# Kernel optimization log

Measured on AMD Instinct MI355X. Metric: run time of the kernel, lower is better.

Reference implementation:

```python
import jax, jax.numpy as jnp
import numpy as np

N, L, S, E, A, D = 16, 256, 128, 128, 9, 768
ARG_ROLES = 23      # score width = ARG_ROLES + 1
MAX_ARG = 9         # hard-coded max_len_arg in the torch module
N_HID = 768


def setup_inputs() -> dict:
    key = jax.random.key(0)
    ks = jax.random.split(key, 10)
    all_embeddings = jax.random.normal(ks[0], (N, L, D), jnp.float32)
    # last-3-layer BERT attention maps, 12 heads, positive entries
    attn_last3 = jax.random.uniform(ks[1], (3, N, 12, L, L), jnp.float32)
    # per-sample sorted distinct first-subword indices (all positive, full length:
    # the ragged filter idxs>0 then keeps everything -> fixed-shape gather)
    idx_keys = jax.random.split(ks[2], N)
    cand = jnp.arange(1, L - MAX_ARG - 1)
    idxs_to_collect = jax.vmap(
        lambda k: jnp.sort(jax.random.choice(k, cand, (S + 2,), replace=False))
    )(idx_keys).astype(jnp.int32)
    is_triggers = (jax.random.uniform(ks[3], (N, S)) < 0.05).astype(jnp.float32)
    is_triggers = is_triggers.at[:, 0].set(1.0)  # >=1 trigger per sample
    entity_mapping = jax.random.normal(ks[4], (N, S, E), jnp.float32) * 0.05
    arg_weight_matrices = jax.random.normal(ks[5], (N, MAX_ARG, A), jnp.float32) * 0.3
    map_keys = jax.random.split(ks[6], N)
    arg_mapping = jax.vmap(
        lambda k: jax.random.permutation(k, ARG_ROLES + 1)[:A]
    )(map_keys).astype(jnp.int32)
    W1 = jax.random.normal(ks[7], (6 * D, N_HID), jnp.float32) * 0.02
    b1 = jnp.zeros((N_HID,), jnp.float32)
    W2 = jax.random.normal(ks[8], (N_HID, 1), jnp.float32) * 0.02
    b2 = jnp.zeros((1,), jnp.float32)
    return {
        "all_embeddings": all_embeddings,
        "attn_last3": attn_last3,
        "entity_mapping": entity_mapping,
        "arg_weight_matrices": arg_weight_matrices,
        "is_triggers": is_triggers,
        "W1": W1, "b1": b1, "W2": W2, "b2": b2,
        "idxs_to_collect": idxs_to_collect,
        "arg_mapping": arg_mapping,
    }


def reference(all_embeddings, attn_last3, entity_mapping, arg_weight_matrices,
              is_triggers, W1, b1, W2, b2, idxs_to_collect, arg_mapping):
    sqrt_d = jnp.sqrt(jnp.asarray(D, jnp.float32))
    sent_idx = idxs_to_collect[:, :S]                      # [N,S] first-subword ids
    # get_fist_subword_embeddings: ragged gather (full-length here)
    sent_emb = jnp.take_along_axis(all_embeddings, sent_idx[:, :, None], axis=1)  # [N,S,D]
    # arg-type tokens sit right after the second-to-last [SEP]
    arg_pos = idxs_to_collect[:, -2:-1] + 1 + jnp.arange(MAX_ARG)[None, :]        # [N,9]
    arg_raw = jnp.take_along_axis(all_embeddings, arg_pos[:, :, None], axis=1)    # [N,9,D]

    entity_emb = jnp.einsum('nsd,nse->ned', sent_emb, entity_mapping)             # [N,E,D]
    trig = jnp.sum(sent_emb * is_triggers[..., None], axis=1) \
           / jnp.sum(is_triggers, axis=1, keepdims=True)                          # [N,D]
    del trig  # _trigger is computed but unused downstream in the torch forward
    arg_emb = jnp.einsum('nkd,nka->nad', arg_raw, arg_weight_matrices)            # [N,A,D]

    # bi-attention scores (broadcast-mul-sum == contraction over D)
    t2a = jnp.einsum('ned,nad->nea', entity_emb, arg_emb) / sqrt_d
    w = (t2a - 5.0) / 2.0                                                         # [N,E,A]
    token_argAwared = jnp.einsum('nea,nad->ned', w, arg_emb)                      # [N,E,D]
    arg_tokenAwared = jnp.einsum('nea,ned->nad', w, entity_emb)                   # [N,A,D]

    # select_hidden_att for each of the last 3 layers
    att_mean = jnp.mean(attn_last3, axis=2)                                       # [3,N,L,L]
    def sel_layer(a):  # a: [N,L,L] -> row/col gather + row renorm
        s = jax.vmap(lambda m, i: m[i][:, i])(a, sent_idx)                        # [N,S,S]
        return s / (jnp.sum(s, axis=-1, keepdims=True) + 1e-9)
    t2t = (sel_layer(att_mean[0]) + sel_layer(att_mean[1]) + sel_layer(att_mean[2])) / 3.0

    h2h_sent = jnp.einsum('nst,ntd->nsd', t2t, sent_emb)                          # [N,S,D]
    # A_h2h and H_ are projected from sent space (S) to entity space (E)
    A_h2h_e = jnp.einsum('nsd,nse->ned', h2h_sent, entity_mapping)                # [N,E,D]
    H_e = entity_emb                                                              # sent_emb projected == entity_emb

    a2a = jax.nn.softmax(jnp.einsum('nad,nbd->nab', arg_emb, arg_emb), axis=-1)   # [N,A,A]
    u2u = jnp.einsum('nab,nbd->nad', a2a, arg_emb)                                # [N,A,D]

    shp = (N, E, A, D)
    H_    = jnp.broadcast_to(H_e[:, :, None, :], shp)
    U_    = jnp.broadcast_to(arg_emb[:, None, :, :], shp)
    A_h2u = jnp.broadcast_to(token_argAwared[:, :, None, :], shp)
    A_h2h = jnp.broadcast_to(A_h2h_e[:, :, None, :], shp)
    A_u2h = jnp.broadcast_to(arg_tokenAwared[:, None, :, :], shp)
    A_u2u = jnp.broadcast_to(u2u[:, None, :, :], shp)
    latent = jnp.concatenate([H_, U_, A_h2u, A_h2h, A_u2h, A_u2u], axis=-1)       # [N,E,A,6D]

    hid = jax.nn.gelu(latent @ W1 + b1, approximate=False)                        # [N,E,A,768]
    score = (hid @ W2 + b2)[..., 0]                                               # [N,E,A]

    # map_arg_to_ids: scatter each arg slot back to its global role id
    def scatter_one(s, ids):  # s [E,A], ids [A]
        return jnp.full((E, ARG_ROLES + 1), -1e6, jnp.float32).at[:, ids].set(s)
    new_score = jax.vmap(scatter_one)(score, arg_mapping)                         # [N,E,24]
    return new_score
```

## Files before the change

kernel.cpp:

```cpp
#include <hip/hip_runtime.h>
#include <math.h>

namespace {
constexpr int N_ = 16, L_ = 256, S_ = 128, E_ = 128, A_ = 9, D_ = 768, H_ = 768, RO_ = 24;
constexpr int IDXW = 130;
constexpr int W1R = 6 * D_;
constexpr float INV_SQRT_D = 0.03608439182435161f;
}

using bshort8 = __attribute__((ext_vector_type(8))) short;
using f32x4v = __attribute__((ext_vector_type(4))) float;

__device__ __forceinline__ unsigned short f2bf(float f) {
    unsigned u = __builtin_bit_cast(unsigned, f);
    return (unsigned short)((u + 0x7fffu + ((u >> 16) & 1u)) >> 16);
}

__global__ __launch_bounds__(256) void zero2_k(float* __restrict__ Pe, float* __restrict__ Pa) {
    const int i = blockIdx.x * 256 + threadIdx.x;
    const float4 z = {0.f, 0.f, 0.f, 0.f};
    if (i < (N_ * E_ * H_) / 4) reinterpret_cast<float4*>(Pe)[i] = z;
    if (i < (N_ * A_ * H_) / 4) reinterpret_cast<float4*>(Pa)[i] = z;
}

__global__ __launch_bounds__(256) void gatherT_k(const float* __restrict__ all_emb,
                                                 const int* __restrict__ idxs,
                                                 unsigned short* __restrict__ sentT) {
    const int n = blockIdx.x, d0 = blockIdx.y * 64;
    __shared__ unsigned short tile[64][132];
#pragma unroll
    for (int it = 0; it < 8; ++it) {
        const int lin = threadIdx.x + 256 * it;
        const int s = lin >> 4, dq = (lin & 15) * 4;
        const int row = idxs[n * IDXW + s];
        const float4 v = *reinterpret_cast<const float4*>(all_emb + ((size_t)(n * L_ + row)) * D_ + d0 + dq);
        tile[dq + 0][s] = f2bf(v.x); tile[dq + 1][s] = f2bf(v.y);
        tile[dq + 2][s] = f2bf(v.z); tile[dq + 3][s] = f2bf(v.w);
    }
    __syncthreads();
#pragma unroll
    for (int it = 0; it < 8; ++it) {
        const int lin = threadIdx.x + 256 * it;
        const int d = lin >> 5, s4 = (lin & 31) * 4;
        ushort4 v = {tile[d][s4], tile[d][s4 + 1], tile[d][s4 + 2], tile[d][s4 + 3]};
        *reinterpret_cast<ushort4*>(sentT + ((size_t)(n * D_) + d0 + d) * S_ + s4) = v;
    }
}

__global__ __launch_bounds__(256) void entmapT_k(const float* __restrict__ ent_map,
                                                 unsigned short* __restrict__ entmapT) {
    const int n = blockIdx.x;
    __shared__ unsigned short tile[128][132];
#pragma unroll
    for (int it = 0; it < 16; ++it) {
        const int lin = threadIdx.x + 256 * it;
        const int s = lin >> 5, eq = (lin & 31) * 4;
        const float4 v = *reinterpret_cast<const float4*>(ent_map + ((size_t)(n * S_ + s)) * E_ + eq);
        tile[eq + 0][s] = f2bf(v.x); tile[eq + 1][s] = f2bf(v.y);
        tile[eq + 2][s] = f2bf(v.z); tile[eq + 3][s] = f2bf(v.w);
    }
    __syncthreads();
#pragma unroll
    for (int it = 0; it < 16; ++it) {
        const int lin = threadIdx.x + 256 * it;
        const int e = lin >> 5, s4 = (lin & 31) * 4;
        ushort4 v = {tile[e][s4], tile[e][s4 + 1], tile[e][s4 + 2], tile[e][s4 + 3]};
        *reinterpret_cast<ushort4*>(entmapT + ((size_t)(n * E_) + e) * S_ + s4) = v;
    }
}

__global__ __launch_bounds__(256) void transpose_w1_k(const float* __restrict__ W1, short* __restrict__ W1t) {
    __shared__ float tile[64][65];
    const int k0 = blockIdx.x * 64, h0 = blockIdx.y * 64;
    const int tx = threadIdx.x & 63, ty = threadIdx.x >> 6;
#pragma unroll
    for (int i = 0; i < 16; ++i) {
        const int r = ty + i * 4;
        tile[r][tx] = W1[(size_t)(k0 + r) * H_ + h0 + tx];
    }
    __syncthreads();
#pragma unroll
    for (int i = 0; i < 16; ++i) {
        const int r = ty + i * 4;
        W1t[(size_t)(h0 + r) * W1R + k0 + tx] = (short)f2bf(tile[tx][r]);
    }
}

__global__ __launch_bounds__(128) void t2t_k(const float* __restrict__ attn,
                                             const int* __restrict__ idxs,
                                             unsigned short* __restrict__ t2tbf) {
    const int n = blockIdx.x >> 7, s = blockIdx.x & 127;
    const int t = threadIdx.x;
    const int w = t >> 6, lane = t & 63;
    const int is = idxs[n * IDXW + s], it = idxs[n * IDXW + t];
    __shared__ float sum2[3][2][256];
    __shared__ float part[3][2];
#pragma unroll
    for (int l = 0; l < 3; ++l) {
        const float* base = attn + ((size_t)((l * N_ + n) * 12 + w * 6)) * (L_ * L_)
                          + (size_t)is * L_ + lane * 4;
        float4 acc = {0.f, 0.f, 0.f, 0.f};
#pragma unroll
        for (int h = 0; h < 6; ++h) {
            const float4 v = *reinterpret_cast<const float4*>(base + (size_t)h * (L_ * L_));
            acc.x += v.x; acc.y += v.y; acc.z += v.z; acc.w += v.w;
        }
        *reinterpret_cast<float4*>(&sum2[l][w][lane * 4]) = acc;
    }
    __syncthreads();
    float m[3];
#pragma unroll
    for (int l = 0; l < 3; ++l) {
        m[l] = (sum2[l][0][it] + sum2[l][1][it]) * (1.0f / 12.0f);
        float r = m[l];
#pragma unroll
        for (int off = 32; off; off >>= 1) r += __shfl_xor(r, off, 64);
        if (lane == 0) part[l][w] = r;
    }
    __syncthreads();
    float out = 0.f;
#pragma unroll
    for (int l = 0; l < 3; ++l)
        out += m[l] / (part[l][0] + part[l][1] + 1e-9f);
    t2tbf[((size_t)(n * S_ + s)) * S_ + t] = f2bf(out * (1.0f / 3.0f));
}

__global__ __launch_bounds__(256) void arg_u2u_k(const float* __restrict__ all_emb,
                                                 const int* __restrict__ idxs,
                                                 const float* __restrict__ argw,
                                                 float* __restrict__ argE,
                                                 unsigned short* __restrict__ argEbf,
                                                 unsigned short* __restrict__ u2ubf) {
    const int n = blockIdx.x, tid = threadIdx.x;
    __shared__ float wsm[A_][A_];
    __shared__ float part[45][4];
    __shared__ float Psm[A_][A_];
    if (tid < A_ * A_) wsm[tid / A_][tid % A_] = argw[n * A_ * A_ + tid];
    __syncthreads();
    const int p0 = idxs[n * IDXW + S_] + 1;
    float pp[45] = {};
    float vals[3][A_];
#pragma unroll
    for (int c = 0; c < 3; ++c) {
        const int d = tid + 256 * c;
        float raw[A_];
#pragma unroll
        for (int k = 0; k < A_; ++k) raw[k] = all_emb[((size_t)(n * L_ + p0 + k)) * D_ + d];
#pragma unroll
        for (int a = 0; a < A_; ++a) {
            float acc = 0.f;
#pragma unroll
            for (int k = 0; k < A_; ++k) acc = fmaf(raw[k], wsm[k][a], acc);
            vals[c][a] = acc;
            argE[((size_t)(n * A_ + a)) * D_ + d] = acc;
            argEbf[((size_t)(n * A_ + a)) * D_ + d] = f2bf(acc);
        }
        int p = 0;
#pragma unroll
        for (int a = 0; a < A_; ++a)
#pragma unroll
            for (int b = a; b < A_; ++b) pp[p++] += vals[c][a] * vals[c][b];
    }
    const int lane = tid & 63, wv = tid >> 6;
#pragma unroll
    for (int p = 0; p < 45; ++p) {
        float v = pp[p];
        for (int off = 32; off; off >>= 1) v += __shfl_down(v, off, 64);
        if (lane == 0) part[p][wv] = v;
    }
    __syncthreads();
    if (tid < 45) part[tid][0] = part[tid][0] + part[tid][1] + part[tid][2] + part[tid][3];
    __syncthreads();
    if (tid < A_) {
        const int a = tid;
        float v[A_], mx = -1e30f;
#pragma unroll
        for (int b = 0; b < A_; ++b) {
            const int lo = a < b ? a : b, hi = a < b ? b : a;
            v[b] = part[lo * (19 - lo) / 2 + hi - lo][0];
            mx = fmaxf(mx, v[b]);
        }
        float s = 0.f;
#pragma unroll
        for (int b = 0; b < A_; ++b) { v[b] = expf(v[b] - mx); s += v[b]; }
        const float inv = 1.0f / s;
#pragma unroll
        for (int b = 0; b < A_; ++b) Psm[a][b] = v[b] * inv;
    }
    __syncthreads();
#pragma unroll
    for (int c = 0; c < 3; ++c) {
        const int d = tid + 256 * c;
#pragma unroll
        for (int a = 0; a < A_; ++a) {
            float acc = 0.f;
#pragma unroll
            for (int b = 0; b < A_; ++b) acc = fmaf(Psm[a][b], vals[c][b], acc);
            u2ubf[((size_t)(n * A_ + a)) * D_ + d] = f2bf(acc);
        }
    }
}

template <int MODE>
__global__ __launch_bounds__(256) void gemm128_k(const unsigned short* __restrict__ Ab,
                                                 const unsigned short* __restrict__ BTb,
                                                 float* __restrict__ Cf,
                                                 unsigned short* __restrict__ Cb) {
    __shared__ __align__(16) short As[128][40];
    __shared__ __align__(16) short Bs[64][40];
    const int n = blockIdx.y, c0 = blockIdx.x * 64;
    const unsigned short* A = Ab + (size_t)n * S_ * S_;
    const unsigned short* BT = BTb + (size_t)n * D_ * S_;
    const int tid = threadIdx.x;
    const int wave = tid >> 6, lane = tid & 63;
    const int row16 = lane & 15, quad = lane >> 4;
    f32x4v acc[2][4] = {};
    for (int k0 = 0; k0 < S_; k0 += 32) {
#pragma unroll
        for (int i = 0; i < 2; ++i) {
            const int idx = tid + 256 * i;
            const int r = idx >> 2, q = idx & 3;
            *reinterpret_cast<bshort8*>(&As[r][q * 8]) =
                *reinterpret_cast<const bshort8*>(A + (size_t)r * S_ + k0 + q * 8);
        }
        {
            const int col = tid >> 2, q = tid & 3;
            *reinterpret_cast<bshort8*>(&Bs[col][q * 8]) =
                *reinterpret_cast<const bshort8*>(BT + (size_t)(c0 + col) * S_ + k0 + q * 8);
        }
        __syncthreads();
        bshort8 a[2], b[4];
#pragma unroll
        for (int mi = 0; mi < 2; ++mi)
            a[mi] = *reinterpret_cast<const bshort8*>(&As[wave * 32 + mi * 16 + row16][quad * 8]);
#pragma unroll
        for (int ni = 0; ni < 4; ++ni)
            b[ni] = *reinterpret_cast<const bshort8*>(&Bs[ni * 16 + row16][quad * 8]);
#pragma unroll
        for (int mi = 0; mi < 2; ++mi)
#pragma unroll
            for (int ni = 0; ni < 4; ++ni)
                acc[mi][ni] = __builtin_amdgcn_mfma_f32_16x16x32_bf16(a[mi], b[ni], acc[mi][ni], 0, 0, 0);
        __syncthreads();
    }
#pragma unroll
    for (int mi = 0; mi < 2; ++mi) {
#pragma unroll
        for (int ni = 0; ni < 4; ++ni) {
            const int rbase = wave * 32 + mi * 16 + quad * 4;
            const int col = c0 + ni * 16 + row16;
            if (MODE == 1) {
                ushort4 v = {f2bf(acc[mi][ni][0]), f2bf(acc[mi][ni][1]),
                             f2bf(acc[mi][ni][2]), f2bf(acc[mi][ni][3])};
                *reinterpret_cast<ushort4*>(Cb + (size_t)n * D_ * S_ + (size_t)col * S_ + rbase) = v;
            } else {
#pragma unroll
                for (int t = 0; t < 4; ++t) {
                    const size_t o = ((size_t)n * S_ + rbase + t) * D_ + col;
                    Cb[o] = f2bf(acc[mi][ni][t]);
                }
            }
        }
    }
}

__global__ __launch_bounds__(256) void gemm_pair_k(const unsigned short* __restrict__ t2tbf,
                                                   const unsigned short* __restrict__ entmapT,
                                                   const unsigned short* __restrict__ sentT,
                                                   float* __restrict__ entf,
                                                   unsigned short* __restrict__ entbf,
                                                   unsigned short* __restrict__ h2hT) {
    __shared__ __align__(16) short As[128][40];
    __shared__ __align__(16) short Bs[64][40];
    const int n = blockIdx.y, c0 = blockIdx.x * 64, z = blockIdx.z;
    const unsigned short* A = (z == 0 ? t2tbf : entmapT) + (size_t)n * S_ * S_;
    const unsigned short* BT = sentT + (size_t)n * D_ * S_;
    const int tid = threadIdx.x;
    const int wave = tid >> 6, lane = tid & 63;
    const int row16 = lane & 15, quad = lane >> 4;
    f32x4v acc[2][4] = {};
    for (int k0 = 0; k0 < S_; k0 += 32) {
#pragma unroll
        for (int i = 0; i < 2; ++i) {
            const int idx = tid + 256 * i;
            const int r = idx >> 2, q = idx & 3;
            *reinterpret_cast<bshort8*>(&As[r][q * 8]) =
                *reinterpret_cast<const bshort8*>(A + (size_t)r * S_ + k0 + q * 8);
        }
        {
            const int col = tid >> 2, q = tid & 3;
            *reinterpret_cast<bshort8*>(&Bs[col][q * 8]) =
                *reinterpret_cast<const bshort8*>(BT + (size_t)(c0 + col) * S_ + k0 + q * 8);
        }
        __syncthreads();
        bshort8 a[2], b[4];
#pragma unroll
        for (int mi = 0; mi < 2; ++mi)
            a[mi] = *reinterpret_cast<const bshort8*>(&As[wave * 32 + mi * 16 + row16][quad * 8]);
#pragma unroll
        for (int ni = 0; ni < 4; ++ni)
            b[ni] = *reinterpret_cast<const bshort8*>(&Bs[ni * 16 + row16][quad * 8]);
#pragma unroll
        for (int mi = 0; mi < 2; ++mi)
#pragma unroll
            for (int ni = 0; ni < 4; ++ni)
                acc[mi][ni] = __builtin_amdgcn_mfma_f32_16x16x32_bf16(a[mi], b[ni], acc[mi][ni], 0, 0, 0);
        __syncthreads();
    }
#pragma unroll
    for (int mi = 0; mi < 2; ++mi) {
#pragma unroll
        for (int ni = 0; ni < 4; ++ni) {
            const int rbase = wave * 32 + mi * 16 + quad * 4;
            const int col = c0 + ni * 16 + row16;
            if (z == 0) {
                ushort4 v = {f2bf(acc[mi][ni][0]), f2bf(acc[mi][ni][1]),
                             f2bf(acc[mi][ni][2]), f2bf(acc[mi][ni][3])};
                *reinterpret_cast<ushort4*>(h2hT + (size_t)n * D_ * S_ + (size_t)col * S_ + rbase) = v;
            } else {
#pragma unroll
                for (int t = 0; t < 4; ++t) {
                    const size_t o = ((size_t)n * S_ + rbase + t) * D_ + col;
                    entf[o] = acc[mi][ni][t];
                    entbf[o] = f2bf(acc[mi][ni][t]);
                }
            }
        }
    }
}

__global__ __launch_bounds__(256) void w_tokA_k(const float* __restrict__ ent, const float* __restrict__ argE,
                                                float* __restrict__ wbuf, unsigned short* __restrict__ tokAbf) {
    const int n = blockIdx.x >> 7, e = blockIdx.x & 127;
    const int tid = threadIdx.x;
    const float* er = ent + ((size_t)(n * E_ + e)) * D_;
    const float* ar = argE + (size_t)n * A_ * D_;
    float acc[A_] = {};
    for (int d = tid; d < D_; d += 256) {
        const float ev = er[d];
#pragma unroll
        for (int a = 0; a < A_; ++a) acc[a] = fmaf(ev, ar[(size_t)a * D_ + d], acc[a]);
    }
    const int lane = tid & 63, wv = tid >> 6;
#pragma unroll
    for (int a = 0; a < A_; ++a)
        for (int off = 32; off; off >>= 1) acc[a] += __shfl_down(acc[a], off, 64);
    __shared__ float part[A_][4];
    __shared__ float wl[A_];
    if (lane == 0)
        for (int a = 0; a < A_; ++a) part[a][wv] = acc[a];
    __syncthreads();
    if (tid < A_) {
        const float s = part[tid][0] + part[tid][1] + part[tid][2] + part[tid][3];
        const float w = (s * INV_SQRT_D - 5.0f) * 0.5f;
        wl[tid] = w;
        wbuf[(size_t)(n * E_ + e) * A_ + tid] = w;
    }
    __syncthreads();
    for (int d = tid; d < D_; d += 256) {
        float s = 0.f;
#pragma unroll
        for (int a = 0; a < A_; ++a) s = fmaf(wl[a], ar[(size_t)a * D_ + d], s);
        tokAbf[((size_t)(n * E_ + e)) * D_ + d] = f2bf(s);
    }
}

__global__ __launch_bounds__(256) void argT_k(const float* __restrict__ wbuf, const float* __restrict__ ent,
                                              unsigned short* __restrict__ argTbf) {
    const int n = blockIdx.x / A_, a = blockIdx.x % A_;
    const int tid = threadIdx.x;
    __shared__ float wl[E_];
    if (tid < E_) wl[tid] = wbuf[(size_t)(n * E_ + tid) * A_ + a];
    __syncthreads();
    const float* eb = ent + (size_t)n * E_ * D_;
    for (int d = tid; d < D_; d += 256) {
        float acc = 0.f;
        for (int e = 0; e < E_; ++e) acc = fmaf(wl[e], eb[(size_t)e * D_ + d], acc);
        argTbf[((size_t)(n * A_ + a)) * D_ + d] = f2bf(acc);
    }
}

__global__ __launch_bounds__(256) void mfma_mlp_k(const unsigned short* __restrict__ e0,
                                                  const unsigned short* __restrict__ e1,
                                                  const unsigned short* __restrict__ e2,
                                                  const unsigned short* __restrict__ a0,
                                                  const unsigned short* __restrict__ a1,
                                                  const unsigned short* __restrict__ a2,
                                                  const short* __restrict__ W1t,
                                                  float* __restrict__ Pe, float* __restrict__ Pa) {
    __shared__ __align__(16) short As[128][40];
    __shared__ __align__(16) short Bs[64][40];
    const int bx = blockIdx.x;
    const int seg = bx % 3;
    const int blk = bx / 3;
    const bool isPa = blk >= 16;
    const unsigned short* Aseg;
    int woff;
    if (isPa) {
        Aseg = seg == 0 ? a0 : (seg == 1 ? a1 : a2);
        woff = seg == 0 ? 1 * D_ : (seg == 1 ? 4 * D_ : 5 * D_);
    } else {
        Aseg = seg == 0 ? e0 : (seg == 1 ? e1 : e2);
        woff = seg == 0 ? 0 : (seg == 1 ? 2 * D_ : 3 * D_);
    }
    const int M = isPa ? N_ * A_ : N_ * E_;
    const int r0 = (isPa ? blk - 16 : blk) * 128;
    float* C = isPa ? Pa : Pe;
    const int c0 = blockIdx.y * 64;
    const int tid = threadIdx.x;
    const int wave = tid >> 6, lane = tid & 63;
    const int row16 = lane & 15, quad = lane >> 4;
    f32x4v acc[2][4] = {};
    for (int kk = 0; kk < D_; kk += 32) {
#pragma unroll
        for (int i = 0; i < 2; ++i) {
            const int idx = tid + 256 * i;
            const int r = idx >> 2, q = idx & 3;
            bshort8 av = {};
            if (r0 + r < M) av = *reinterpret_cast<const bshort8*>(Aseg + (size_t)(r0 + r) * D_ + kk + q * 8);
            *reinterpret_cast<bshort8*>(&As[r][q * 8]) = av;
        }
        {
            const int col = tid >> 2, q = tid & 3;
            *reinterpret_cast<bshort8*>(&Bs[col][q * 8]) =
                *reinterpret_cast<const bshort8*>(W1t + (size_t)(c0 + col) * W1R + woff + kk + q * 8);
        }
        __syncthreads();
        bshort8 a[2], b[4];
#pragma unroll
        for (int mi = 0; mi < 2; ++mi)
            a[mi] = *reinterpret_cast<const bshort8*>(&As[wave * 32 + mi * 16 + row16][quad * 8]);
#pragma unroll
        for (int ni = 0; ni < 4; ++ni)
            b[ni] = *reinterpret_cast<const bshort8*>(&Bs[ni * 16 + row16][quad * 8]);
#pragma unroll
        for (int mi = 0; mi < 2; ++mi)
#pragma unroll
            for (int ni = 0; ni < 4; ++ni)
                acc[mi][ni] = __builtin_amdgcn_mfma_f32_16x16x32_bf16(a[mi], b[ni], acc[mi][ni], 0, 0, 0);
        __syncthreads();
    }
#pragma unroll
    for (int mi = 0; mi < 2; ++mi) {
#pragma unroll
        for (int ni = 0; ni < 4; ++ni) {
            const int rbase = r0 + wave * 32 + mi * 16 + quad * 4;
            const int col = c0 + ni * 16 + row16;
#pragma unroll
            for (int t = 0; t < 4; ++t)
                if (rbase + t < M) atomicAdd(&C[(size_t)(rbase + t) * H_ + col], acc[mi][ni][t]);
        }
    }
}

__global__ __launch_bounds__(256) void score_k(const float* __restrict__ Pe, const float* __restrict__ Pa,
                                               const float* __restrict__ b1, const float* __restrict__ W2,
                                               const float* __restrict__ b2, const int* __restrict__ arg_map,
                                               float* __restrict__ out) {
    const int n = blockIdx.x >> 7, e = blockIdx.x & 127;
    const int tid = threadIdx.x;
    __shared__ float paS[A_ * H_];
    __shared__ float part[A_][4];
    float* orow = out + ((size_t)(n * E_ + e)) * RO_;
    if (tid < RO_) orow[tid] = -1000000.0f;
    for (int i = tid; i < A_ * H_; i += 256) paS[i] = Pa[(size_t)n * A_ * H_ + i];
    __syncthreads();
    const float* per = Pe + ((size_t)(n * E_ + e)) * H_;
    float acc[A_] = {};
    for (int h = tid; h < H_; h += 256) {
        const float pe = per[h] + b1[h];
        const float w2 = W2[h];
#pragma unroll
        for (int a = 0; a < A_; ++a) {
            const float x = pe + paS[a * H_ + h];
            const float g = x * 0.5f * (1.0f + erff(x * 0.70710678118654752f));
            acc[a] = fmaf(g, w2, acc[a]);
        }
    }
    const int lane = tid & 63, wv = tid >> 6;
#pragma unroll
    for (int a = 0; a < A_; ++a)
        for (int off = 32; off; off >>= 1) acc[a] += __shfl_down(acc[a], off, 64);
    if (lane == 0)
        for (int a = 0; a < A_; ++a) part[a][wv] = acc[a];
    __syncthreads();
    if (tid < A_) {
        const float s = part[tid][0] + part[tid][1] + part[tid][2] + part[tid][3] + b2[0];
        orow[arg_map[n * A_ + tid]] = s;
    }
}

extern "C" void kernel_launch(void* const* d_in, const int* in_sizes, int n_in,
                              void* d_out, int out_size, void* d_ws, size_t ws_size,
                              hipStream_t stream) {
    const float* all_emb = (const float*)d_in[0];
    const float* attn    = (const float*)d_in[1];
    const float* ent_map = (const float*)d_in[2];
    const float* argw    = (const float*)d_in[3];
    const float* W1 = (const float*)d_in[5];
    const float* b1 = (const float*)d_in[6];
    const float* W2 = (const float*)d_in[7];
    const float* b2 = (const float*)d_in[8];
    const int* idxs    = (const int*)d_in[9];
    const int* arg_map = (const int*)d_in[10];
    float* out = (float*)d_out;

    float* ws = (float*)d_ws;
    float* entf = ws + 0;
    float* Pe   = ws + 1572864;
    float* argE = ws + 3145728;
    float* wbuf = ws + 3256320;
    float* Pa   = ws + 3274752;
    short*          W1t     = (short*)(ws + 3385344);
    unsigned short* sentT   = (unsigned short*)(ws + 5154816);
    unsigned short* entmapT = (unsigned short*)(ws + 5941248);
    unsigned short* t2tbf   = (unsigned short*)(ws + 6072320);
    unsigned short* argEbf  = (unsigned short*)(ws + 6127616);
    unsigned short* u2ubf   = (unsigned short*)(ws + 6182912);
    unsigned short* entbf   = (unsigned short*)(ws + 6238208);
    unsigned short* h2hT    = (unsigned short*)(ws + 7024640);
    unsigned short* Ah2hbf  = (unsigned short*)(ws + 7811072);
    unsigned short* tokAbf  = (unsigned short*)(ws + 8597504);
    unsigned short* argTbf  = (unsigned short*)(ws + 9383936);

    zero2_k<<<(N_ * E_ * H_) / 4 / 256, 256, 0, stream>>>(Pe, Pa);

    gatherT_k<<<dim3(N_, D_ / 64), 256, 0, stream>>>(all_emb, idxs, sentT);
    entmapT_k<<<N_, 256, 0, stream>>>(ent_map, entmapT);
    transpose_w1_k<<<dim3(W1R / 64, H_ / 64), 256, 0, stream>>>(W1, W1t);
    t2t_k<<<N_ * S_, 128, 0, stream>>>(attn, idxs, t2tbf);
    arg_u2u_k<<<N_, 256, 0, stream>>>(all_emb, idxs, argw, argE, argEbf, u2ubf);

    gemm_pair_k<<<dim3(D_ / 64, N_, 2), 256, 0, stream>>>(t2tbf, entmapT, sentT, entf, entbf, h2hT);
    gemm128_k<2><<<dim3(D_ / 64, N_), 256, 0, stream>>>(entmapT, h2hT, nullptr, Ah2hbf);

    w_tokA_k<<<N_ * E_, 256, 0, stream>>>(entf, argE, wbuf, tokAbf);
    argT_k<<<N_ * A_, 256, 0, stream>>>(wbuf, entf, argTbf);

    mfma_mlp_k<<<dim3(54, H_ / 64), 256, 0, stream>>>(entbf, tokAbf, Ah2hbf, argEbf, argTbf, u2ubf, W1t, Pe, Pa);

    score_k<<<N_ * E_, 256, 0, stream>>>(Pe, Pa, b1, W2, b2, arg_map, out);

    (void)in_sizes; (void)n_in; (void)out_size; (void)ws_size;
}
```

Measured before the change: 350.7 us.

## Merge preprocessing kernels into one launch and replace atomics with per-segment partials

New measurement: 318.2 us. 1.1x faster.

```diff
diff --git a/kernel.cpp b/kernel.cpp
--- a/kernel.cpp
+++ b/kernel.cpp
@@ -6,6 +6,14 @@
 constexpr int IDXW = 130;
 constexpr int W1R = 6 * D_;
 constexpr float INV_SQRT_D = 0.03608439182435161f;
+constexpr int PESZ = 2048 * 768;
+constexpr int PASZ = 144 * 768;
+constexpr int GB_GATHER = 0;
+constexpr int GB_ENTMAP = 192;
+constexpr int GB_W1T    = 208;
+constexpr int GB_T2T    = 1072;
+constexpr int GB_ARGU   = 2096;
+constexpr int GB_TOTAL  = 2112;
 }
 
 using bshort8 = __attribute__((ext_vector_type(8))) short;
@@ -16,249 +24,182 @@
     return (unsigned short)((u + 0x7fffu + ((u >> 16) & 1u)) >> 16);
 }
 
-__global__ __launch_bounds__(256) void zero2_k(float* __restrict__ Pe, float* __restrict__ Pa) {
-    const int i = blockIdx.x * 256 + threadIdx.x;
-    const float4 z = {0.f, 0.f, 0.f, 0.f};
-    if (i < (N_ * E_ * H_) / 4) reinterpret_cast<float4*>(Pe)[i] = z;
-    if (i < (N_ * A_ * H_) / 4) reinterpret_cast<float4*>(Pa)[i] = z;
-}
-
-__global__ __launch_bounds__(256) void gatherT_k(const float* __restrict__ all_emb,
-                                                 const int* __restrict__ idxs,
-                                                 unsigned short* __restrict__ sentT) {
-    const int n = blockIdx.x, d0 = blockIdx.y * 64;
-    __shared__ unsigned short tile[64][132];
-#pragma unroll
-    for (int it = 0; it < 8; ++it) {
-        const int lin = threadIdx.x + 256 * it;
-        const int s = lin >> 4, dq = (lin & 15) * 4;
-        const int row = idxs[n * IDXW + s];
-        const float4 v = *reinterpret_cast<const float4*>(all_emb + ((size_t)(n * L_ + row)) * D_ + d0 + dq);
-        tile[dq + 0][s] = f2bf(v.x); tile[dq + 1][s] = f2bf(v.y);
-        tile[dq + 2][s] = f2bf(v.z); tile[dq + 3][s] = f2bf(v.w);
-    }
-    __syncthreads();
-#pragma unroll
-    for (int it = 0; it < 8; ++it) {
-        const int lin = threadIdx.x + 256 * it;
-        const int d = lin >> 5, s4 = (lin & 31) * 4;
-        ushort4 v = {tile[d][s4], tile[d][s4 + 1], tile[d][s4 + 2], tile[d][s4 + 3]};
-        *reinterpret_cast<ushort4*>(sentT + ((size_t)(n * D_) + d0 + d) * S_ + s4) = v;
-    }
-}
-
-__global__ __launch_bounds__(256) void entmapT_k(const float* __restrict__ ent_map,
-                                                 unsigned short* __restrict__ entmapT) {
-    const int n = blockIdx.x;
-    __shared__ unsigned short tile[128][132];
-#pragma unroll
-    for (int it = 0; it < 16; ++it) {
-        const int lin = threadIdx.x + 256 * it;
-        const int s = lin >> 5, eq = (lin & 31) * 4;
-        const float4 v = *reinterpret_cast<const float4*>(ent_map + ((size_t)(n * S_ + s)) * E_ + eq);
-        tile[eq + 0][s] = f2bf(v.x); tile[eq + 1][s] = f2bf(v.y);
-        tile[eq + 2][s] = f2bf(v.z); tile[eq + 3][s] = f2bf(v.w);
-    }
-    __syncthreads();
-#pragma unroll
-    for (int it = 0; it < 16; ++it) {
-        const int lin = threadIdx.x + 256 * it;
-        const int e = lin >> 5, s4 = (lin & 31) * 4;
-        ushort4 v = {tile[e][s4], tile[e][s4 + 1], tile[e][s4 + 2], tile[e][s4 + 3]};
-        *reinterpret_cast<ushort4*>(entmapT + ((size_t)(n * E_) + e) * S_ + s4) = v;
-    }
-}
-
-__global__ __launch_bounds__(256) void transpose_w1_k(const float* __restrict__ W1, short* __restrict__ W1t) {
-    __shared__ float tile[64][65];
-    const int k0 = blockIdx.x * 64, h0 = blockIdx.y * 64;
-    const int tx = threadIdx.x & 63, ty = threadIdx.x >> 6;
-#pragma unroll
-    for (int i = 0; i < 16; ++i) {
-        const int r = ty + i * 4;
-        tile[r][tx] = W1[(size_t)(k0 + r) * H_ + h0 + tx];
-    }
-    __syncthreads();
-#pragma unroll
-    for (int i = 0; i < 16; ++i) {
-        const int r = ty + i * 4;
-        W1t[(size_t)(h0 + r) * W1R + k0 + tx] = (short)f2bf(tile[tx][r]);
-    }
-}
-
-__global__ __launch_bounds__(128) void t2t_k(const float* __restrict__ attn,
-                                             const int* __restrict__ idxs,
-                                             unsigned short* __restrict__ t2tbf) {
-    const int n = blockIdx.x >> 7, s = blockIdx.x & 127;
-    const int t = threadIdx.x;
-    const int w = t >> 6, lane = t & 63;
-    const int is = idxs[n * IDXW + s], it = idxs[n * IDXW + t];
-    __shared__ float sum2[3][2][256];
-    __shared__ float part[3][2];
-#pragma unroll
-    for (int l = 0; l < 3; ++l) {
-        const float* base = attn + ((size_t)((l * N_ + n) * 12 + w * 6)) * (L_ * L_)
-                          + (size_t)is * L_ + lane * 4;
-        float4 acc = {0.f, 0.f, 0.f, 0.f};
-#pragma unroll
-        for (int h = 0; h < 6; ++h) {
-            const float4 v = *reinterpret_cast<const float4*>(base + (size_t)h * (L_ * L_));
-            acc.x += v.x; acc.y += v.y; acc.z += v.z; acc.w += v.w;
-        }
-        *reinterpret_cast<float4*>(&sum2[l][w][lane * 4]) = acc;
-    }
-    __syncthreads();
-    float m[3];
-#pragma unroll
-    for (int l = 0; l < 3; ++l) {
-        m[l] = (sum2[l][0][it] + sum2[l][1][it]) * (1.0f / 12.0f);
-        float r = m[l];
-#pragma unroll
-        for (int off = 32; off; off >>= 1) r += __shfl_xor(r, off, 64);
-        if (lane == 0) part[l][w] = r;
-    }
-    __syncthreads();
-    float out = 0.f;
-#pragma unroll
-    for (int l = 0; l < 3; ++l)
-        out += m[l] / (part[l][0] + part[l][1] + 1e-9f);
-    t2tbf[((size_t)(n * S_ + s)) * S_ + t] = f2bf(out * (1.0f / 3.0f));
-}
-
-__global__ __launch_bounds__(256) void arg_u2u_k(const float* __restrict__ all_emb,
-                                                 const int* __restrict__ idxs,
-                                                 const float* __restrict__ argw,
-                                                 float* __restrict__ argE,
-                                                 unsigned short* __restrict__ argEbf,
-                                                 unsigned short* __restrict__ u2ubf) {
-    const int n = blockIdx.x, tid = threadIdx.x;
-    __shared__ float wsm[A_][A_];
-    __shared__ float part[45][4];
-    __shared__ float Psm[A_][A_];
-    if (tid < A_ * A_) wsm[tid / A_][tid % A_] = argw[n * A_ * A_ + tid];
-    __syncthreads();
-    const int p0 = idxs[n * IDXW + S_] + 1;
-    float pp[45] = {};
-    float vals[3][A_];
-#pragma unroll
-    for (int c = 0; c < 3; ++c) {
-        const int d = tid + 256 * c;
-        float raw[A_];
-#pragma unroll
-        for (int k = 0; k < A_; ++k) raw[k] = all_emb[((size_t)(n * L_ + p0 + k)) * D_ + d];
-#pragma unroll
-        for (int a = 0; a < A_; ++a) {
-            float acc = 0.f;
-#pragma unroll
-            for (int k = 0; k < A_; ++k) acc = fmaf(raw[k], wsm[k][a], acc);
-            vals[c][a] = acc;
-            argE[((size_t)(n * A_ + a)) * D_ + d] = acc;
-            argEbf[((size_t)(n * A_ + a)) * D_ + d] = f2bf(acc);
-        }
-        int p = 0;
-#pragma unroll
-        for (int a = 0; a < A_; ++a)
-#pragma unroll
-            for (int b = a; b < A_; ++b) pp[p++] += vals[c][a] * vals[c][b];
-    }
-    const int lane = tid & 63, wv = tid >> 6;
-#pragma unroll
-    for (int p = 0; p < 45; ++p) {
-        float v = pp[p];
-        for (int off = 32; off; off >>= 1) v += __shfl_down(v, off, 64);
-        if (lane == 0) part[p][wv] = v;
-    }
-    __syncthreads();
-    if (tid < 45) part[tid][0] = part[tid][0] + part[tid][1] + part[tid][2] + part[tid][3];
-    __syncthreads();
-    if (tid < A_) {
-        const int a = tid;
-        float v[A_], mx = -1e30f;
-#pragma unroll
-        for (int b = 0; b < A_; ++b) {
-            const int lo = a < b ? a : b, hi = a < b ? b : a;
-            v[b] = part[lo * (19 - lo) / 2 + hi - lo][0];
-            mx = fmaxf(mx, v[b]);
-        }
-        float s = 0.f;
-#pragma unroll
-        for (int b = 0; b < A_; ++b) { v[b] = expf(v[b] - mx); s += v[b]; }
-        const float inv = 1.0f / s;
-#pragma unroll
-        for (int b = 0; b < A_; ++b) Psm[a][b] = v[b] * inv;
-    }
-    __syncthreads();
-#pragma unroll
-    for (int c = 0; c < 3; ++c) {
-        const int d = tid + 256 * c;
-#pragma unroll
-        for (int a = 0; a < A_; ++a) {
-            float acc = 0.f;
-#pragma unroll
-            for (int b = 0; b < A_; ++b) acc = fmaf(Psm[a][b], vals[c][b], acc);
-            u2ubf[((size_t)(n * A_ + a)) * D_ + d] = f2bf(acc);
-        }
-    }
-}
-
-template <int MODE>
-__global__ __launch_bounds__(256) void gemm128_k(const unsigned short* __restrict__ Ab,
-                                                 const unsigned short* __restrict__ BTb,
-                                                 float* __restrict__ Cf,
-                                                 unsigned short* __restrict__ Cb) {
-    __shared__ __align__(16) short As[128][40];
-    __shared__ __align__(16) short Bs[64][40];
-    const int n = blockIdx.y, c0 = blockIdx.x * 64;
-    const unsigned short* A = Ab + (size_t)n * S_ * S_;
-    const unsigned short* BT = BTb + (size_t)n * D_ * S_;
-    const int tid = threadIdx.x;
-    const int wave = tid >> 6, lane = tid & 63;
-    const int row16 = lane & 15, quad = lane >> 4;
-    f32x4v acc[2][4] = {};
-    for (int k0 = 0; k0 < S_; k0 += 32) {
-#pragma unroll
-        for (int i = 0; i < 2; ++i) {
-            const int idx = tid + 256 * i;
-            const int r = idx >> 2, q = idx & 3;
-            *reinterpret_cast<bshort8*>(&As[r][q * 8]) =
-                *reinterpret_cast<const bshort8*>(A + (size_t)r * S_ + k0 + q * 8);
-        }
-        {
-            const int col = tid >> 2, q = tid & 3;
-            *reinterpret_cast<bshort8*>(&Bs[col][q * 8]) =
-                *reinterpret_cast<const bshort8*>(BT + (size_t)(c0 + col) * S_ + k0 + q * 8);
-        }
-        __syncthreads();
-        bshort8 a[2], b[4];
-#pragma unroll
-        for (int mi = 0; mi < 2; ++mi)
-            a[mi] = *reinterpret_cast<const bshort8*>(&As[wave * 32 + mi * 16 + row16][quad * 8]);
-#pragma unroll
-        for (int ni = 0; ni < 4; ++ni)
-            b[ni] = *reinterpret_cast<const bshort8*>(&Bs[ni * 16 + row16][quad * 8]);
-#pragma unroll
-        for (int mi = 0; mi < 2; ++mi)
-#pragma unroll
-            for (int ni = 0; ni < 4; ++ni)
-                acc[mi][ni] = __builtin_amdgcn_mfma_f32_16x16x32_bf16(a[mi], b[ni], acc[mi][ni], 0, 0, 0);
-        __syncthreads();
-    }
-#pragma unroll
-    for (int mi = 0; mi < 2; ++mi) {
-#pragma unroll
-        for (int ni = 0; ni < 4; ++ni) {
-            const int rbase = wave * 32 + mi * 16 + quad * 4;
-            const int col = c0 + ni * 16 + row16;
-            if (MODE == 1) {
-                ushort4 v = {f2bf(acc[mi][ni][0]), f2bf(acc[mi][ni][1]),
-                             f2bf(acc[mi][ni][2]), f2bf(acc[mi][ni][3])};
-                *reinterpret_cast<ushort4*>(Cb + (size_t)n * D_ * S_ + (size_t)col * S_ + rbase) = v;
-            } else {
-#pragma unroll
-                for (int t = 0; t < 4; ++t) {
-                    const size_t o = ((size_t)n * S_ + rbase + t) * D_ + col;
-                    Cb[o] = f2bf(acc[mi][ni][t]);
-                }
+__global__ __launch_bounds__(256) void stage1_k(const float* __restrict__ all_emb,
+                                                const int* __restrict__ idxs,
+                                                const float* __restrict__ ent_map,
+                                                const float* __restrict__ W1,
+                                                const float* __restrict__ argw,
+                                                const float* __restrict__ attn,
+                                                unsigned short* __restrict__ sentT,
+                                                unsigned short* __restrict__ entmapT,
+                                                short* __restrict__ W1t,
+                                                unsigned short* __restrict__ t2tbf,
+                                                float* __restrict__ argE,
+                                                unsigned short* __restrict__ argEbf,
+                                                unsigned short* __restrict__ u2ubf) {
+    __shared__ __align__(16) unsigned char smem[33792];
+    const int b = blockIdx.x, tid = threadIdx.x;
+
+    if (b < GB_ENTMAP) {
+        const int n = b / 12, d0 = (b % 12) * 64;
+        auto tile = (unsigned short (*)[132])smem;
+#pragma unroll
+        for (int it = 0; it < 8; ++it) {
+            const int lin = tid + 256 * it;
+            const int s = lin >> 4, dq = (lin & 15) * 4;
+            const int row = idxs[n * IDXW + s];
+            const float4 v = *reinterpret_cast<const float4*>(all_emb + ((size_t)(n * L_ + row)) * D_ + d0 + dq);
+            tile[dq + 0][s] = f2bf(v.x); tile[dq + 1][s] = f2bf(v.y);
+            tile[dq + 2][s] = f2bf(v.z); tile[dq + 3][s] = f2bf(v.w);
+        }
+        __syncthreads();
+#pragma unroll
+        for (int it = 0; it < 8; ++it) {
+            const int lin = tid + 256 * it;
+            const int d = lin >> 5, s4 = (lin & 31) * 4;
+            ushort4 v = {tile[d][s4], tile[d][s4 + 1], tile[d][s4 + 2], tile[d][s4 + 3]};
+            *reinterpret_cast<ushort4*>(sentT + ((size_t)(n * D_) + d0 + d) * S_ + s4) = v;
+        }
+    } else if (b < GB_W1T) {
+        const int n = b - GB_ENTMAP;
+        auto tile = (unsigned short (*)[132])smem;
+#pragma unroll
+        for (int it = 0; it < 16; ++it) {
+            const int lin = tid + 256 * it;
+            const int s = lin >> 5, eq = (lin & 31) * 4;
+            const float4 v = *reinterpret_cast<const float4*>(ent_map + ((size_t)(n * S_ + s)) * E_ + eq);
+            tile[eq + 0][s] = f2bf(v.x); tile[eq + 1][s] = f2bf(v.y);
+            tile[eq + 2][s] = f2bf(v.z); tile[eq + 3][s] = f2bf(v.w);
+        }
+        __syncthreads();
+#pragma unroll
+        for (int it = 0; it < 16; ++it) {
+            const int lin = tid + 256 * it;
+            const int e = lin >> 5, s4 = (lin & 31) * 4;
+            ushort4 v = {tile[e][s4], tile[e][s4 + 1], tile[e][s4 + 2], tile[e][s4 + 3]};
+            *reinterpret_cast<ushort4*>(entmapT + ((size_t)(n * E_) + e) * S_ + s4) = v;
+        }
+    } else if (b < GB_T2T) {
+        const int b2 = b - GB_W1T;
+        const int k0 = (b2 % 72) * 64, h0 = (b2 / 72) * 64;
+        auto tile = (float (*)[65])smem;
+        const int tx = tid & 63, ty = tid >> 6;
+#pragma unroll
+        for (int i = 0; i < 16; ++i) {
+            const int r = ty + i * 4;
+            tile[r][tx] = W1[(size_t)(k0 + r) * H_ + h0 + tx];
+        }
+        __syncthreads();
+#pragma unroll
+        for (int i = 0; i < 16; ++i) {
+            const int r = ty + i * 4;
+            W1t[(size_t)(h0 + r) * W1R + k0 + tx] = (short)f2bf(tile[tx][r]);
+        }
+    } else if (b < GB_ARGU) {
+        const int idx = b - GB_T2T;
+        const int n = idx >> 6;
+        const int half = tid >> 7, t128 = tid & 127;
+        const int s = ((idx & 63) << 1) | half;
+        const int w = t128 >> 6, lane = tid & 63;
+        float* sum2 = (float*)smem;
+        float* part = (float*)(smem + 12288);
+        const int is = idxs[n * IDXW + s], it = idxs[n * IDXW + t128];
+#pragma unroll
+        for (int l = 0; l < 3; ++l) {
+            const float* base = attn + ((size_t)((l * N_ + n) * 12 + w * 6)) * (L_ * L_)
+                              + (size_t)is * L_ + lane * 4;
+            float4 acc = {0.f, 0.f, 0.f, 0.f};
+#pragma unroll
+            for (int h = 0; h < 6; ++h) {
+                const float4 v = *reinterpret_cast<const float4*>(base + (size_t)h * (L_ * L_));
+                acc.x += v.x; acc.y += v.y; acc.z += v.z; acc.w += v.w;
+            }
+            *reinterpret_cast<float4*>(&sum2[(((half * 3 + l) * 2 + w) << 8) + lane * 4]) = acc;
+        }
+        __syncthreads();
+        float m[3];
+#pragma unroll
+        for (int l = 0; l < 3; ++l) {
+            m[l] = (sum2[(((half * 3 + l) * 2 + 0) << 8) + it] +
+                    sum2[(((half * 3 + l) * 2 + 1) << 8) + it]) * (1.0f / 12.0f);
+            float r = m[l];
+#pragma unroll
+            for (int off = 32; off; off >>= 1) r += __shfl_xor(r, off, 64);
+            if (lane == 0) part[(half * 3 + l) * 2 + w] = r;
+        }
+        __syncthreads();
+        float out = 0.f;
+#pragma unroll
+        for (int l = 0; l < 3; ++l)
+            out += m[l] / (part[(half * 3 + l) * 2 + 0] + part[(half * 3 + l) * 2 + 1] + 1e-9f);
+        t2tbf[((size_t)(n * S_ + s)) * S_ + t128] = f2bf(out * (1.0f / 3.0f));
+    } else {
+        const int n = b - GB_ARGU;
+        auto wsm = (float (*)[A_])smem;
+        auto part45 = (float (*)[4])(smem + 512);
+        auto Psm = (float (*)[A_])(smem + 1536);
+        if (tid < A_ * A_) wsm[tid / A_][tid % A_] = argw[n * A_ * A_ + tid];
+        __syncthreads();
+        const int p0 = idxs[n * IDXW + S_] + 1;
+        float pp[45] = {};
+        float vals[3][A_];
+#pragma unroll
+        for (int c = 0; c < 3; ++c) {
+            const int d = tid + 256 * c;
+            float raw[A_];
+#pragma unroll
+            for (int k = 0; k < A_; ++k) raw[k] = all_emb[((size_t)(n * L_ + p0 + k)) * D_ + d];
+#pragma unroll
+            for (int a = 0; a < A_; ++a) {
+                float acc = 0.f;
+#pragma unroll
+                for (int k = 0; k < A_; ++k) acc = fmaf(raw[k], wsm[k][a], acc);
+                vals[c][a] = acc;
+                argE[((size_t)(n * A_ + a)) * D_ + d] = acc;
+                argEbf[((size_t)(n * A_ + a)) * D_ + d] = f2bf(acc);
+            }
+            int p = 0;
+#pragma unroll
+            for (int a = 0; a < A_; ++a)
+#pragma unroll
+                for (int bb = a; bb < A_; ++bb) pp[p++] += vals[c][a] * vals[c][bb];
+        }
+        const int lane = tid & 63, wv = tid >> 6;
+#pragma unroll
+        for (int p = 0; p < 45; ++p) {
+            float v = pp[p];
+            for (int off = 32; off; off >>= 1) v += __shfl_down(v, off, 64);
+            if (lane == 0) part45[p][wv] = v;
+        }
+        __syncthreads();
+        if (tid < 45) part45[tid][0] = part45[tid][0] + part45[tid][1] + part45[tid][2] + part45[tid][3];
+        __syncthreads();
+        if (tid < A_) {
+            const int a = tid;
+            float v[A_], mx = -1e30f;
+#pragma unroll
+            for (int bb = 0; bb < A_; ++bb) {
+                const int lo = a < bb ? a : bb, hi = a < bb ? bb : a;
+                v[bb] = part45[lo * (19 - lo) / 2 + hi - lo][0];
+                mx = fmaxf(mx, v[bb]);
+            }
+            float sm = 0.f;
+#pragma unroll
+            for (int bb = 0; bb < A_; ++bb) { v[bb] = expf(v[bb] - mx); sm += v[bb]; }
+            const float inv = 1.0f / sm;
+#pragma unroll
+            for (int bb = 0; bb < A_; ++bb) Psm[a][bb] = v[bb] * inv;
+        }
+        __syncthreads();
+#pragma unroll
+        for (int c = 0; c < 3; ++c) {
+            const int d = tid + 256 * c;
+#pragma unroll
+            for (int a = 0; a < A_; ++a) {
+                float acc = 0.f;
+#pragma unroll
+                for (int bb = 0; bb < A_; ++bb) acc = fmaf(Psm[a][bb], vals[c][bb], acc);
+                u2ubf[((size_t)(n * A_ + a)) * D_ + d] = f2bf(acc);
             }
         }
     }
@@ -329,54 +270,122 @@
     }
 }
 
-__global__ __launch_bounds__(256) void w_tokA_k(const float* __restrict__ ent, const float* __restrict__ argE,
-                                                float* __restrict__ wbuf, unsigned short* __restrict__ tokAbf) {
-    const int n = blockIdx.x >> 7, e = blockIdx.x & 127;
-    const int tid = threadIdx.x;
-    const float* er = ent + ((size_t)(n * E_ + e)) * D_;
-    const float* ar = argE + (size_t)n * A_ * D_;
-    float acc[A_] = {};
-    for (int d = tid; d < D_; d += 256) {
-        const float ev = er[d];
-#pragma unroll
-        for (int a = 0; a < A_; ++a) acc[a] = fmaf(ev, ar[(size_t)a * D_ + d], acc[a]);
-    }
-    const int lane = tid & 63, wv = tid >> 6;
-#pragma unroll
-    for (int a = 0; a < A_; ++a)
-        for (int off = 32; off; off >>= 1) acc[a] += __shfl_down(acc[a], off, 64);
-    __shared__ float part[A_][4];
-    __shared__ float wl[A_];
-    if (lane == 0)
-        for (int a = 0; a < A_; ++a) part[a][wv] = acc[a];
-    __syncthreads();
-    if (tid < A_) {
-        const float s = part[tid][0] + part[tid][1] + part[tid][2] + part[tid][3];
-        const float w = (s * INV_SQRT_D - 5.0f) * 0.5f;
-        wl[tid] = w;
-        wbuf[(size_t)(n * E_ + e) * A_ + tid] = w;
-    }
-    __syncthreads();
-    for (int d = tid; d < D_; d += 256) {
-        float s = 0.f;
-#pragma unroll
-        for (int a = 0; a < A_; ++a) s = fmaf(wl[a], ar[(size_t)a * D_ + d], s);
-        tokAbf[((size_t)(n * E_ + e)) * D_ + d] = f2bf(s);
-    }
-}
-
-__global__ __launch_bounds__(256) void argT_k(const float* __restrict__ wbuf, const float* __restrict__ ent,
+__global__ __launch_bounds__(256) void gemm2_k(const unsigned short* __restrict__ entmapT,
+                                               const unsigned short* __restrict__ h2hT,
+                                               const unsigned short* __restrict__ entbf,
+                                               const unsigned short* __restrict__ argEbf,
+                                               unsigned short* __restrict__ Ah2hbf,
+                                               float* __restrict__ wbuf) {
+    const int bx = blockIdx.x, tid = threadIdx.x;
+    const int wave = tid >> 6, lane = tid & 63;
+    const int row16 = lane & 15, quad = lane >> 4;
+    if (bx < 192) {
+        __shared__ __align__(16) short As[128][40];
+        __shared__ __align__(16) short Bs[64][40];
+        const int n = bx / 12, c0 = (bx % 12) * 64;
+        const unsigned short* A = entmapT + (size_t)n * S_ * S_;
+        const unsigned short* BT = h2hT + (size_t)n * D_ * S_;
+        f32x4v acc[2][4] = {};
+        for (int k0 = 0; k0 < S_; k0 += 32) {
+#pragma unroll
+            for (int i = 0; i < 2; ++i) {
+                const int idx = tid + 256 * i;
+                const int r = idx >> 2, q = idx & 3;
+                *reinterpret_cast<bshort8*>(&As[r][q * 8]) =
+                    *reinterpret_cast<const bshort8*>(A + (size_t)r * S_ + k0 + q * 8);
+            }
+            {
+                const int col = tid >> 2, q = tid & 3;
+                *reinterpret_cast<bshort8*>(&Bs[col][q * 8]) =
+                    *reinterpret_cast<const bshort8*>(BT + (size_t)(c0 + col) * S_ + k0 + q * 8);
+            }
+            __syncthreads();
+            bshort8 a[2], b[4];
+#pragma unroll
+            for (int mi = 0; mi < 2; ++mi)
+                a[mi] = *reinterpret_cast<const bshort8*>(&As[wave * 32 + mi * 16 + row16][quad * 8]);
+#pragma unroll
+            for (int ni = 0; ni < 4; ++ni)
+                b[ni] = *reinterpret_cast<const bshort8*>(&Bs[ni * 16 + row16][quad * 8]);
+#pragma unroll
+            for (int mi = 0; mi < 2; ++mi)
+#pragma unroll
+                for (int ni = 0; ni < 4; ++ni)
+                    acc[mi][ni] = __builtin_amdgcn_mfma_f32_16x16x32_bf16(a[mi], b[ni], acc[mi][ni], 0, 0, 0);
+            __syncthreads();
+        }
+#pragma unroll
+        for (int mi = 0; mi < 2; ++mi)
+#pragma unroll
+            for (int ni = 0; ni < 4; ++ni) {
+                const int rbase = wave * 32 + mi * 16 + quad * 4;
+                const int col = c0 + ni * 16 + row16;
+#pragma unroll
+                for (int t = 0; t < 4; ++t)
+                    Ah2hbf[((size_t)n * S_ + rbase + t) * D_ + col] = f2bf(acc[mi][ni][t]);
+            }
+    } else {
+        const int n = bx - 192;
+        const unsigned short* Aent = entbf + (size_t)n * E_ * D_;
+        const unsigned short* Barg = argEbf + (size_t)n * A_ * D_;
+        f32x4v acc[2] = {};
+        for (int k0 = 0; k0 < D_; k0 += 32) {
+            bshort8 a[2], b;
+#pragma unroll
+            for (int mi = 0; mi < 2; ++mi)
+                a[mi] = *reinterpret_cast<const bshort8*>(Aent + (size_t)(wave * 32 + mi * 16 + row16) * D_ + k0 + quad * 8);
+            b = *reinterpret_cast<const bshort8*>(Barg + (size_t)row16 * D_ + k0 + quad * 8);
+#pragma unroll
+            for (int mi = 0; mi < 2; ++mi)
+                acc[mi] = __builtin_amdgcn_mfma_f32_16x16x32_bf16(a[mi], b, acc[mi], 0, 0, 0);
+        }
+        if (row16 < A_) {
+#pragma unroll
+            for (int mi = 0; mi < 2; ++mi)
+#pragma unroll
+                for (int t = 0; t < 4; ++t) {
+                    const int e = wave * 32 + mi * 16 + quad * 4 + t;
+                    const float w = (acc[mi][t] * INV_SQRT_D - 5.0f) * 0.5f;
+                    wbuf[((size_t)(n * E_ + e)) * A_ + row16] = w;
+                }
+        }
+    }
+}
+
+__global__ __launch_bounds__(256) void post_k(const float* __restrict__ wbuf,
+                                              const float* __restrict__ argE,
+                                              const float* __restrict__ entf,
+                                              unsigned short* __restrict__ tokAbf,
                                               unsigned short* __restrict__ argTbf) {
-    const int n = blockIdx.x / A_, a = blockIdx.x % A_;
-    const int tid = threadIdx.x;
-    __shared__ float wl[E_];
-    if (tid < E_) wl[tid] = wbuf[(size_t)(n * E_ + tid) * A_ + a];
-    __syncthreads();
-    const float* eb = ent + (size_t)n * E_ * D_;
-    for (int d = tid; d < D_; d += 256) {
-        float acc = 0.f;
-        for (int e = 0; e < E_; ++e) acc = fmaf(wl[e], eb[(size_t)e * D_ + d], acc);
-        argTbf[((size_t)(n * A_ + a)) * D_ + d] = f2bf(acc);
+    const int b = blockIdx.x, tid = threadIdx.x;
+    if (b < N_ * E_) {
+        const int n = b >> 7, e = b & 127;
+        __shared__ float wl[A_];
+        if (tid < A_) wl[tid] = wbuf[(size_t)(n * E_ + e) * A_ + tid];
+        __syncthreads();
+        const float* ar = argE + (size_t)n * A_ * D_;
+#pragma unroll
+        for (int c = 0; c < 3; ++c) {
+            const int d = tid + 256 * c;
+            float s = 0.f;
+#pragma unroll
+            for (int a = 0; a < A_; ++a) s = fmaf(wl[a], ar[(size_t)a * D_ + d], s);
+            tokAbf[((size_t)(n * E_ + e)) * D_ + d] = f2bf(s);
+        }
+    } else {
+        const int idx = b - N_ * E_;
+        const int n = idx / A_, a = idx % A_;
+        __shared__ float wl[E_];
+        if (tid < E_) wl[tid] = wbuf[(size_t)(n * E_ + tid) * A_ + a];
+        __syncthreads();
+        const float* eb = entf + (size_t)n * E_ * D_;
+#pragma unroll
+        for (int c = 0; c < 3; ++c) {
+            const int d = tid + 256 * c;
+            float acc = 0.f;
+            for (int e = 0; e < E_; ++e) acc = fmaf(wl[e], eb[(size_t)e * D_ + d], acc);
+            argTbf[((size_t)(n * A_ + a)) * D_ + d] = f2bf(acc);
+        }
     }
 }
 
@@ -387,7 +396,7 @@
                                                   const unsigned short* __restrict__ a1,
                                                   const unsigned short* __restrict__ a2,
                                                   const short* __restrict__ W1t,
-                                                  float* __restrict__ Pe, float* __restrict__ Pa) {
+                                                  float* __restrict__ Pe3, float* __restrict__ Pa3) {
     __shared__ __align__(16) short As[128][40];
     __shared__ __align__(16) short Bs[64][40];
     const int bx = blockIdx.x;
@@ -405,7 +414,7 @@
     }
     const int M = isPa ? N_ * A_ : N_ * E_;
     const int r0 = (isPa ? blk - 16 : blk) * 128;
-    float* C = isPa ? Pa : Pe;
+    float* C = isPa ? (Pa3 + (size_t)seg * PASZ) : (Pe3 + (size_t)seg * PESZ);
     const int c0 = blockIdx.y * 64;
     const int tid = threadIdx.x;
     const int wave = tid >> 6, lane = tid & 63;
@@ -448,12 +457,12 @@
             const int col = c0 + ni * 16 + row16;
 #pragma unroll
             for (int t = 0; t < 4; ++t)
-                if (rbase + t < M) atomicAdd(&C[(size_t)(rbase + t) * H_ + col], acc[mi][ni][t]);
-        }
-    }
-}
-
-__global__ __launch_bounds__(256) void score_k(const float* __restrict__ Pe, const float* __restrict__ Pa,
+                if (rbase + t < M) C[(size_t)(rbase + t) * H_ + col] = acc[mi][ni][t];
+        }
+    }
+}
+
+__global__ __launch_bounds__(256) void score_k(const float* __restrict__ Pe3, const float* __restrict__ Pa3,
                                                const float* __restrict__ b1, const float* __restrict__ W2,
                                                const float* __restrict__ b2, const int* __restrict__ arg_map,
                                                float* __restrict__ out) {
@@ -463,12 +472,15 @@
     __shared__ float part[A_][4];
     float* orow = out + ((size_t)(n * E_ + e)) * RO_;
     if (tid < RO_) orow[tid] = -1000000.0f;
-    for (int i = tid; i < A_ * H_; i += 256) paS[i] = Pa[(size_t)n * A_ * H_ + i];
+    for (int i = tid; i < A_ * H_; i += 256) {
+        const size_t o = (size_t)n * A_ * H_ + i;
+        paS[i] = Pa3[o] + Pa3[PASZ + o] + Pa3[2 * PASZ + o];
+    }
     __syncthreads();
-    const float* per = Pe + ((size_t)(n * E_ + e)) * H_;
+    const size_t ro = ((size_t)(n * E_ + e)) * H_;
     float acc[A_] = {};
     for (int h = tid; h < H_; h += 256) {
-        const float pe = per[h] + b1[h];
+        const float pe = Pe3[ro + h] + Pe3[PESZ + ro + h] + Pe3[2 * PESZ + ro + h] + b1[h];
         const float w2 = W2[h];
 #pragma unroll
         for (int a = 0; a < A_; ++a) {
@@ -507,39 +519,34 @@
 
     float* ws = (float*)d_ws;
     float* entf = ws + 0;
-    float* Pe   = ws + 1572864;
-    float* argE = ws + 3145728;
-    float* wbuf = ws + 3256320;
-    float* Pa   = ws + 3274752;
-    short*          W1t     = (short*)(ws + 3385344);
-    unsigned short* sentT   = (unsigned short*)(ws + 5154816);
-    unsigned short* entmapT = (unsigned short*)(ws + 5941248);
-    unsigned short* t2tbf   = (unsigned short*)(ws + 6072320);
-    unsigned short* argEbf  = (unsigned short*)(ws + 6127616);
-    unsigned short* u2ubf   = (unsigned short*)(ws + 6182912);
-    unsigned short* entbf   = (unsigned short*)(ws + 6238208);
-    unsigned short* h2hT    = (unsigned short*)(ws + 7024640);
-    unsigned short* Ah2hbf  = (unsigned short*)(ws + 7811072);
-    unsigned short* tokAbf  = (unsigned short*)(ws + 8597504);
-    unsigned short* argTbf  = (unsigned short*)(ws + 9383936);
-
-    zero2_k<<<(N_ * E_ * H_) / 4 / 256, 256, 0, stream>>>(Pe, Pa);
-
-    gatherT_k<<<dim3(N_, D_ / 64), 256, 0, stream>>>(all_emb, idxs, sentT);
-    entmapT_k<<<N_, 256, 0, stream>>>(ent_map, entmapT);
-    transpose_w1_k<<<dim3(W1R / 64, H_ / 64), 256, 0, stream>>>(W1, W1t);
-    t2t_k<<<N_ * S_, 128, 0, stream>>>(attn, idxs, t2tbf);
-    arg_u2u_k<<<N_, 256, 0, stream>>>(all_emb, idxs, argw, argE, argEbf, u2ubf);
+    float* Pe3  = ws + 1572864;
+    float* argE = ws + 6291456;
+    float* wbuf = ws + 6402048;
+    float* Pa3  = ws + 6420480;
+    short*          W1t     = (short*)(ws + 6752256);
+    unsigned short* sentT   = (unsigned short*)(ws + 8521728);
+    unsigned short* entmapT = (unsigned short*)(ws + 9308160);
+    unsigned short* t2tbf   = (unsigned short*)(ws + 9439232);
+    unsigned short* argEbf  = (unsigned short*)(ws + 9570304);
+    unsigned short* u2ubf   = (unsigned short*)(ws + 9625600);
+    unsigned short* entbf   = (unsigned short*)(ws + 9680896);
+    unsigned short* h2hT    = (unsigned short*)(ws + 10467328);
+    unsigned short* Ah2hbf  = (unsigned short*)(ws + 11253760);
+    unsigned short* tokAbf  = (unsigned short*)(ws + 12040192);
+    unsigned short* argTbf  = (unsigned short*)(ws + 12826624);
+
+    stage1_k<<<GB_TOTAL, 256, 0, stream>>>(all_emb, idxs, ent_map, W1, argw, attn,
+                                           sentT, entmapT, W1t, t2tbf, argE, argEbf, u2ubf);
 
     gemm_pair_k<<<dim3(D_ / 64, N_, 2), 256, 0, stream>>>(t2tbf, entmapT, sentT, entf, entbf, h2hT);
-    gemm128_k<2><<<dim3(D_ / 64, N_), 256, 0, stream>>>(entmapT, h2hT, nullptr, Ah2hbf);
-
-    w_tokA_k<<<N_ * E_, 256, 0, stream>>>(entf, argE, wbuf, tokAbf);
-    argT_k<<<N_ * A_, 256, 0, stream>>>(wbuf, entf, argTbf);
-
-    mfma_mlp_k<<<dim3(54, H_ / 64), 256, 0, stream>>>(entbf, tokAbf, Ah2hbf, argEbf, argTbf, u2ubf, W1t, Pe, Pa);
-
-    score_k<<<N_ * E_, 256, 0, stream>>>(Pe, Pa, b1, W2, b2, arg_map, out);
+
+    gemm2_k<<<208, 256, 0, stream>>>(entmapT, h2hT, entbf, argEbf, Ah2hbf, wbuf);
+
+    post_k<<<N_ * E_ + N_ * A_, 256, 0, stream>>>(wbuf, argE, entf, tokAbf, argTbf);
+
+    mfma_mlp_k<<<dim3(54, H_ / 64), 256, 0, stream>>>(entbf, tokAbf, Ah2hbf, argEbf, argTbf, u2ubf, W1t, Pe3, Pa3);
+
+    score_k<<<N_ * E_, 256, 0, stream>>>(Pe3, Pa3, b1, W2, b2, arg_map, out);
 
     (void)in_sizes; (void)n_in; (void)out_size; (void)ws_size;
 }
```
